# Kernel optimization log

Measured on AMD Instinct MI355X. Metric: run time of the kernel, lower is better.

Reference implementation:

```python
import jax, jax.numpy as jnp
import numpy as np

B, N, E, D, OUT, L = 4, 10000, 160000, 128, 64, 4
NEG = 0.01  # LeakyReLU slope

def lrelu(x):
    return jnp.where(x > 0, x, NEG * x)

def setup_inputs() -> dict:
    key = jax.random.key(0)
    ks = jax.random.split(key, 20)
    s = 0.05
    inp = {
        "x": jax.random.normal(ks[0], (B, N * 3), dtype=jnp.float32),
        "edge_index": jax.random.randint(ks[1], (2, E), 0, N, dtype=jnp.int32),
        # f0: Linear(3, D)
        "w0": jax.random.normal(ks[2], (3, D), dtype=jnp.float32) * s,
        "b0": jax.random.normal(ks[3], (D,), dtype=jnp.float32) * s,
        # per-layer params stacked on leading L axis
        "ew1": jax.random.normal(ks[4], (L, 2 * D + 1, D), dtype=jnp.float32) * s,
        "eb1": jax.random.normal(ks[5], (L, D), dtype=jnp.float32) * s,
        "ew2": jax.random.normal(ks[6], (L, D, D), dtype=jnp.float32) * s,
        "eb2": jax.random.normal(ks[7], (L, D), dtype=jnp.float32) * s,
        "cw": jax.random.normal(ks[8], (L, D, 1), dtype=jnp.float32) * s,
        "cb": jax.random.normal(ks[9], (L, 1), dtype=jnp.float32) * s,
        "nw1": jax.random.normal(ks[10], (L, 2 * D, D), dtype=jnp.float32) * s,
        "nb1": jax.random.normal(ks[11], (L, D), dtype=jnp.float32) * s,
        "nw2": jax.random.normal(ks[12], (L, D, D), dtype=jnp.float32) * s,
        "nb2": jax.random.normal(ks[13], (L, D), dtype=jnp.float32) * s,
        # project: Linear(D, OUT)
        "wp": jax.random.normal(ks[14], (D, OUT), dtype=jnp.float32) * s,
        "bp": jax.random.normal(ks[15], (OUT,), dtype=jnp.float32) * s,
    }
    return inp

def reference(x, edge_index, w0, b0, ew1, eb1, ew2, eb2, cw, cb, nw1, nb1, nw2, nb2, wp, bp):
    b = x.shape[0]
    n = x.shape[1] // 3
    pos = x.reshape(b, n, 3)            # coordinates [B,N,3]
    h = lrelu(pos @ w0 + b0)            # node features [B,N,D]
    row, col = edge_index[0], edge_index[1]
    # per-node in-edge counts (same for all layers/batches); scatter_mean -> 0 for empty nodes
    cnt = jnp.zeros((n,), x.dtype).at[col].add(1.0)
    denom = jnp.maximum(cnt, 1.0)[None, :, None]
    for i in range(L):
        rel = pos[:, row] - pos[:, col]                          # [B,E,3]
        dist_sq = jnp.sum(rel * rel, axis=-1, keepdims=True)     # [B,E,1]
        edge_in = jnp.concatenate([h[:, row], h[:, col], dist_sq], axis=-1)  # [B,E,2D+1]
        msg = lrelu(lrelu(edge_in @ ew1[i] + eb1[i]) @ ew2[i] + eb2[i])       # [B,E,D]
        aggr = jnp.zeros((b, n, msg.shape[-1]), msg.dtype).at[:, col].add(msg) / denom  # scatter_mean
        coord_update = jnp.tanh(aggr @ cw[i] + cb[i])            # [B,N,1]
        pos = pos + coord_update * 0.1
        node_in = jnp.concatenate([h, aggr], axis=-1)            # [B,N,2D]
        h = h + lrelu(lrelu(node_in @ nw1[i] + nb1[i]) @ nw2[i] + nb2[i])
    return lrelu(h.mean(axis=1) @ wp + bp)                       # [B,OUT]
```

## Files before the change

### kernel.cpp

```cpp
#include <hip/hip_runtime.h>
#include <hip/hip_bf16.h>
#include <math.h>

#define BB   4
#define NN   10000
#define NP   10112
#define EE   160000
#define DD   128
#define OUTD 64
#define LL   4
#define NEGS 0.01f
#define MSTR 136
#define RSF  68

typedef __attribute__((ext_vector_type(8))) short   short8;
typedef __attribute__((ext_vector_type(4))) float   floatx4;
typedef __attribute__((ext_vector_type(4))) uint    uintx4;

__device__ __forceinline__ float lrelu(float x) { return fmaxf(x, NEGS * x); }
__device__ __forceinline__ ushort f2bf(float x) {
    uint u = __builtin_bit_cast(uint, x);
    return (ushort)((u + 0x7FFFu + ((u >> 16) & 1u)) >> 16);
}
__device__ __forceinline__ float bf2f(ushort u) {
    uint v = ((uint)u) << 16;
    return __builtin_bit_cast(float, v);
}
__device__ __forceinline__ float bcf(uint u) { return __builtin_bit_cast(float, u); }

__global__ void k_cvtw_all(const float* __restrict__ ew1, const float* __restrict__ ew2,
                           const float* __restrict__ nw1, const float* __restrict__ nw2,
                           ushort* __restrict__ wtopf, ushort* __restrict__ wmidf,
                           ushort* __restrict__ ew2f, ushort* __restrict__ nw1f,
                           ushort* __restrict__ nw2f) {
    int tid = blockIdx.x * 256 + threadIdx.x;
    const float* src; ushort* dst; int pitch, nks, loc;
    if (tid < 8192)       { src = ew1;                     dst = wtopf; pitch = 257; nks = 4; loc = tid; }
    else if (tid < 16384) { src = ew1 + (size_t)128 * DD;  dst = wmidf; pitch = 257; nks = 4; loc = tid - 8192; }
    else if (tid < 24576) { src = ew2;                     dst = ew2f;  pitch = 128; nks = 4; loc = tid - 16384; }
    else if (tid < 40960) { src = nw1;                     dst = nw1f;  pitch = 256; nks = 8; loc = tid - 24576; }
    else                  { src = nw2;                     dst = nw2f;  pitch = 128; nks = 4; loc = tid - 40960; }
    int lane = loc & 63;
    int nt   = (loc >> 6) & 7;
    int ks   = (loc >> 9) % nks;
    int l    = loc / (nks * 512);
    int quad = lane >> 4, l16 = lane & 15;
    int n = nt * 16 + l16;
    const float* s = src + (size_t)l * pitch * DD;
    ushort* d = dst + (size_t)loc * 8;
    #pragma unroll
    for (int j = 0; j < 8; ++j)
        d[j] = f2bf(s[(size_t)(ks * 32 + quad * 8 + j) * DD + n]);
}

__global__ void k_h0(const float* __restrict__ x, const float* __restrict__ w0,
                     const float* __restrict__ b0, ushort* __restrict__ hb) {
    int idx = blockIdx.x * 256 + threadIdx.x;
    if (idx >= BB * NP * DD) return;
    int d  = idx & (DD - 1);
    int bn = idx >> 7;
    int n  = bn % NP, b = bn / NP;
    float v = 0.0f;
    if (n < NN) {
        const float* p = x + ((size_t)b * NN + n) * 3;
        v = lrelu(b0[d] + p[0] * w0[d] + p[1] * w0[DD + d] + p[2] * w0[2 * DD + d]);
    }
    hb[idx] = f2bf(v);
}

__global__ void k_count(const int* __restrict__ col, float* __restrict__ cnt,
                        int* __restrict__ ecnt) {
    int e = blockIdx.x * blockDim.x + threadIdx.x;
    if (e < EE) {
        int c = col[e];
        atomicAdd(&cnt[c], 1.0f);
        atomicAdd(&ecnt[c], 1);
    }
}

__global__ __launch_bounds__(256) void k_scan(const int* __restrict__ ecnt,
                                              int* __restrict__ cursor) {
    __shared__ int s_sum[256];
    int t = threadIdx.x;
    int base = t * 40;
    int s = 0;
    for (int i = 0; i < 40; ++i) {
        int n = base + i;
        if (n < NN) s += ecnt[n];
    }
    s_sum[t] = s;
    __syncthreads();
    if (t == 0) {
        int a = 0;
        for (int i = 0; i < 256; ++i) { int v = s_sum[i]; s_sum[i] = a; a += v; }
    }
    __syncthreads();
    int a = s_sum[t];
    for (int i = 0; i < 40; ++i) {
        int n = base + i;
        if (n < NN) { cursor[n] = a; a += ecnt[n]; }
    }
}

__global__ void k_place(const int* __restrict__ row, const int* __restrict__ col,
                        int* __restrict__ cursor,
                        int* __restrict__ rowS, int* __restrict__ colS) {
    int e = blockIdx.x * blockDim.x + threadIdx.x;
    if (e >= EE) return;
    int c = col[e];
    int p = atomicAdd(&cursor[c], 1);
    rowS[p] = row[e];
    colS[p] = c;
}

__global__ __launch_bounds__(256) void k_pq(
    const ushort* __restrict__ hb, const ushort* __restrict__ wtf,
    const ushort* __restrict__ wmf, const float* __restrict__ b1,
    ushort* __restrict__ P, ushort* __restrict__ Q)
{
    __shared__ __align__(16) ushort s_out[64 * MSTR];
    const int g = blockIdx.x;
    const int b = (g >> 1) & 3;
    const int n0 = ((g >> 3) * 2 + (g & 1)) * 64;
    const int t = threadIdx.x;
    const int w = t >> 6, lane = t & 63, quad = lane >> 4, l16 = lane & 15;
    const int rw = w * 16;
    const int nw = n0 + rw;

    const ushort* hptr = hb + ((size_t)b * NP + nw + l16) * DD;
    float b1r[8];
    #pragma unroll
    for (int nt = 0; nt < 8; ++nt) b1r[nt] = b1[nt * 16 + l16];

    const short8* wt = (const short8*)wtf;
    const short8* wm = (const short8*)wmf;

    #pragma unroll
    for (int pass = 0; pass < 2; ++pass) {
        floatx4 ap[8];
        #pragma unroll
        for (int nt = 0; nt < 8; ++nt)
            #pragma unroll
            for (int r = 0; r < 4; ++r) ap[nt][r] = pass ? b1r[nt] : 0.0f;
        const short8* wv = pass ? wm : wt;
        #pragma unroll
        for (int ks = 0; ks < 4; ++ks) {
            short8 bf[8];
            #pragma unroll
            for (int nt = 0; nt < 8; ++nt) bf[nt] = wv[(ks * 8 + nt) * 64 + lane];
            short8 af = *(const short8*)(hptr + ks * 32 + quad * 8);
            #pragma unroll
            for (int nt = 0; nt < 8; ++nt)
                ap[nt] = __builtin_amdgcn_mfma_f32_16x16x32_bf16(af, bf[nt], ap[nt], 0, 0, 0);
        }
        #pragma unroll
        for (int nt = 0; nt < 8; ++nt)
            #pragma unroll
            for (int r = 0; r < 4; ++r)
                s_out[(rw + quad * 4 + r) * MSTR + nt * 16 + l16] = f2bf(ap[nt][r]);
        ushort* dst = pass ? Q : P;
        #pragma unroll
        for (int i = 0; i < 4; ++i) {
            int row = rw + i * 4 + quad;
            short8 v = *(const short8*)&s_out[row * MSTR + l16 * 8];
            *(short8*)(dst + ((size_t)b * NP + n0 + row) * DD + l16 * 8) = v;
        }
    }
}

__global__ __launch_bounds__(256, 4) void k_edge(
    const float* __restrict__ pos,
    const ushort* __restrict__ P, const ushort* __restrict__ Q,
    const int* __restrict__ rowS, const int* __restrict__ colS,
    const float* __restrict__ w1last,
    const ushort* __restrict__ w2f, const float* __restrict__ b2,
    float* __restrict__ aggr)
{
    __shared__ int    s_row[128];
    __shared__ int    s_col[128];
    __shared__ float  s_ds[128];
    __shared__ float  s_red[128 * RSF];

    const int g    = blockIdx.x;
    const int b    = (g >> 1) & 3;
    const int tile = (g >> 3) * 2 + (g & 1);
    const int e0   = tile * 128;
    const int t    = threadIdx.x;
    const int w    = t >> 6, lane = t & 63;
    const int quad = lane >> 4, l16 = lane & 15;

    if (t < 128) {
        int e = e0 + t;
        int r = rowS[e], c = colS[e];
        s_row[t] = r;
        s_col[t] = c;
        const float* pr = pos + ((size_t)b * NN + r) * 3;
        const float* pc = pos + ((size_t)b * NN + c) * 3;
        float dx = pr[0] - pc[0], dy = pr[1] - pc[1], dz = pr[2] - pc[2];
        s_ds[t] = dx * dx + dy * dy + dz * dz;
    }
    __syncthreads();

    const int ew = w * 32;
    const ushort* pp[2];
    const ushort* qp[2];
    float dsv[2];
    #pragma unroll
    for (int mt = 0; mt < 2; ++mt) {
        int el = ew + mt * 16 + l16;
        pp[mt]  = P + ((size_t)b * NP + s_row[el]) * DD;
        qp[mt]  = Q + ((size_t)b * NP + s_col[el]) * DD;
        dsv[mt] = s_ds[el];
    }

    uintx4 pf[2][4], qf[2][4];
    #pragma unroll
    for (int ks = 0; ks < 4; ++ks) {
        const int koff = ks * 32 + quad * 8;
        #pragma unroll
        for (int mt = 0; mt < 2; ++mt) {
            pf[mt][ks] = *(const uintx4*)(pp[mt] + koff);
            qf[mt][ks] = *(const uintx4*)(qp[mt] + koff);
        }
    }

    uintx4 mid[2][4];
    #pragma unroll
    for (int ks = 0; ks < 4; ++ks) {
        const int koff = ks * 32 + quad * 8;
        floatx4 wl0 = *(const floatx4*)(w1last + koff);
        floatx4 wl1 = *(const floatx4*)(w1last + koff + 4);
        float wl[8] = {wl0[0], wl0[1], wl0[2], wl0[3], wl1[0], wl1[1], wl1[2], wl1[3]};
        #pragma unroll
        for (int mt = 0; mt < 2; ++mt) {
            #pragma unroll
            for (int i = 0; i < 4; ++i) {
                uint pv = pf[mt][ks][i], qv = qf[mt][ks][i];
                float vlo = lrelu(bcf(pv << 16) + bcf(qv << 16) + dsv[mt] * wl[2 * i]);
                float vhi = lrelu(bcf(pv & 0xFFFF0000u) + bcf(qv & 0xFFFF0000u) + dsv[mt] * wl[2 * i + 1]);
                mid[mt][ks][i] = (__builtin_bit_cast(uint, vlo) >> 16) |
                                 (__builtin_bit_cast(uint, vhi) & 0xFFFF0000u);
            }
        }
    }

    float b2r[8];
    #pragma unroll
    for (int nt = 0; nt < 8; ++nt) b2r[nt] = b2[nt * 16 + l16];

    const short8* w2v = (const short8*)w2f;
    #pragma unroll
    for (int ph = 0; ph < 2; ++ph) {
        floatx4 acc[2][4];
        #pragma unroll
        for (int mt = 0; mt < 2; ++mt)
            #pragma unroll
            for (int ntl = 0; ntl < 4; ++ntl)
                #pragma unroll
                for (int r = 0; r < 4; ++r) acc[mt][ntl][r] = b2r[ph * 4 + ntl];

        #pragma unroll
        for (int ks = 0; ks < 4; ++ks) {
            short8 bf[4];
            #pragma unroll
            for (int ntl = 0; ntl < 4; ++ntl)
                bf[ntl] = w2v[(ks * 8 + ph * 4 + ntl) * 64 + lane];
            #pragma unroll
            for (int mt = 0; mt < 2; ++mt) {
                short8 af = __builtin_bit_cast(short8, mid[mt][ks]);
                #pragma unroll
                for (int ntl = 0; ntl < 4; ++ntl)
                    acc[mt][ntl] = __builtin_amdgcn_mfma_f32_16x16x32_bf16(af, bf[ntl], acc[mt][ntl], 0, 0, 0);
            }
        }

        #pragma unroll
        for (int mt = 0; mt < 2; ++mt)
            #pragma unroll
            for (int ntl = 0; ntl < 4; ++ntl)
                #pragma unroll
                for (int r = 0; r < 4; ++r)
                    s_red[(ew + mt * 16 + quad * 4 + r) * RSF + ntl * 16 + l16] =
                        lrelu(acc[mt][ntl][r]);

        const int d = ph * 64 + lane;
        float run = 0.0f;
        int prev = s_col[ew];
        for (int r = 0; r < 32; ++r) {
            int cid = s_col[ew + r];
            float v = s_red[(ew + r) * RSF + lane];
            if (cid != prev) {
                atomicAdd(&aggr[((size_t)b * NP + prev) * DD + d], run);
                run = 0.0f;
                prev = cid;
            }
            run += v;
        }
        atomicAdd(&aggr[((size_t)b * NP + prev) * DD + d], run);
    }
}

__global__ __launch_bounds__(256) void k_node(
    ushort* hb, float* aggr, const float* __restrict__ cnt,
    const float* __restrict__ cw, const float* __restrict__ cb,
    const ushort* __restrict__ w1f, const float* __restrict__ b1,
    const ushort* __restrict__ w2f, const float* __restrict__ b2,
    float* __restrict__ pos,
    int do_pq,
    const ushort* __restrict__ wtn, const ushort* __restrict__ wmn,
    const float* __restrict__ b1n,
    ushort* __restrict__ P, ushort* __restrict__ Q)
{
    __shared__ __align__(16) ushort s_mid[64 * MSTR];
    __shared__ __align__(16) ushort s_ho[64 * MSTR];

    const int g    = blockIdx.x;
    const int b    = (g >> 1) & 3;
    const int n0   = ((g >> 3) * 2 + (g & 1)) * 64;
    const int t    = threadIdx.x;
    const int w    = t >> 6, lane = t & 63;
    const int quad = lane >> 4, l16 = lane & 15;
    const int rw   = w * 16;
    const int nw   = n0 + rw;

    #pragma unroll
    for (int i = 0; i < 4; ++i) {
        int row = rw + i * 4 + quad;
        short8 v = *(const short8*)(hb + ((size_t)b * NP + n0 + row) * DD + l16 * 8);
        *(short8*)&s_ho[row * MSTR + l16 * 8] = v;
    }

    float* aptr = aggr + ((size_t)b * NP + nw + l16) * DD;
    float inv = 0.0f;
    {
        int node = nw + l16;
        if (node < NN) { float dn = cnt[node]; inv = 1.0f / fmaxf(dn, 1.0f); }
    }
    float b1r[8], b2r[8];
    #pragma unroll
    for (int nt = 0; nt < 8; ++nt) {
        int d = nt * 16 + l16;
        b1r[nt] = b1[d]; b2r[nt] = b2[d];
    }

    floatx4 acc[8];
    #pragma unroll
    for (int nt = 0; nt < 8; ++nt)
        #pragma unroll
        for (int r = 0; r < 4; ++r) acc[nt][r] = b1r[nt];

    float cwacc = 0.0f;
    const floatx4 zero4 = {0.0f, 0.0f, 0.0f, 0.0f};
    const short8* w1v = (const short8*)w1f;
    #pragma unroll
    for (int ks = 0; ks < 8; ++ks) {
        short8 bf[8];
        #pragma unroll
        for (int nt = 0; nt < 8; ++nt) bf[nt] = w1v[(ks * 8 + nt) * 64 + lane];
        const int koff = (ks & 3) * 32 + quad * 8;
        if (ks < 4) {
            short8 af = *(const short8*)(&s_ho[(rw + l16) * MSTR + koff]);
            #pragma unroll
            for (int nt = 0; nt < 8; ++nt)
                acc[nt] = __builtin_amdgcn_mfma_f32_16x16x32_bf16(af, bf[nt], acc[nt], 0, 0, 0);
        } else {
            floatx4 cw0 = *(const floatx4*)(cw + koff);
            floatx4 cw1 = *(const floatx4*)(cw + koff + 4);
            floatx4 a0 = *(const floatx4*)(aptr + koff);
            floatx4 a1 = *(const floatx4*)(aptr + koff + 4);
            *(floatx4*)(aptr + koff)     = zero4;
            *(floatx4*)(aptr + koff + 4) = zero4;
            short8 af;
            #pragma unroll
            for (int j = 0; j < 4; ++j) {
                float v = a0[j] * inv;
                af[j] = (short)f2bf(v);
                cwacc += v * cw0[j];
            }
            #pragma unroll
            for (int j = 0; j < 4; ++j) {
                float v = a1[j] * inv;
                af[4 + j] = (short)f2bf(v);
                cwacc += v * cw1[j];
            }
            #pragma unroll
            for (int nt = 0; nt < 8; ++nt)
                acc[nt] = __builtin_amdgcn_mfma_f32_16x16x32_bf16(af, bf[nt], acc[nt], 0, 0, 0);
        }
    }

    {
        float full = cwacc;
        full += __shfl_xor(full, 16);
        full += __shfl_xor(full, 32);
        int node = nw + l16;
        if (quad == 0 && node < NN) {
            float cu = 0.1f * tanhf(full + cb[0]);
            float* pp = pos + ((size_t)b * NN + node) * 3;
            pp[0] += cu; pp[1] += cu; pp[2] += cu;
        }
    }

    #pragma unroll
    for (int nt = 0; nt < 8; ++nt)
        #pragma unroll
        for (int r = 0; r < 4; ++r)
            s_mid[(rw + quad * 4 + r) * MSTR + nt * 16 + l16] = f2bf(lrelu(acc[nt][r]));

    floatx4 acc2[8];
    #pragma unroll
    for (int nt = 0; nt < 8; ++nt)
        #pragma unroll
        for (int r = 0; r < 4; ++r) acc2[nt][r] = b2r[nt];

    const short8* w2v = (const short8*)w2f;
    #pragma unroll
    for (int ks = 0; ks < 4; ++ks) {
        short8 bf[8];
        #pragma unroll
        for (int nt = 0; nt < 8; ++nt) bf[nt] = w2v[(ks * 8 + nt) * 64 + lane];
        short8 af = *(const short8*)(&s_mid[(rw + l16) * MSTR + ks * 32 + quad * 8]);
        #pragma unroll
        for (int nt = 0; nt < 8; ++nt)
            acc2[nt] = __builtin_amdgcn_mfma_f32_16x16x32_bf16(af, bf[nt], acc2[nt], 0, 0, 0);
    }

    #pragma unroll
    for (int nt = 0; nt < 8; ++nt)
        #pragma unroll
        for (int r = 0; r < 4; ++r) {
            int row = rw + quad * 4 + r;
            float hold = bf2f(s_ho[row * MSTR + nt * 16 + l16]);
            float hv = hold + lrelu(acc2[nt][r]);
            s_mid[row * MSTR + nt * 16 + l16] = f2bf(hv);
        }

    #pragma unroll
    for (int i = 0; i < 4; ++i) {
        int row = rw + i * 4 + quad;
        int n = n0 + row;
        short8 v = *(const short8*)&s_mid[row * MSTR + l16 * 8];
        if (n < NN)
            *(short8*)(hb + ((size_t)b * NP + n) * DD + l16 * 8) = v;
    }

    if (do_pq) {
        const short8* wt = (const short8*)wtn;
        const short8* wm = (const short8*)wmn;
        float b1nr[8];
        #pragma unroll
        for (int nt = 0; nt < 8; ++nt) b1nr[nt] = b1n[nt * 16 + l16];

        #pragma unroll
        for (int pass = 0; pass < 2; ++pass) {
            floatx4 ap[8];
            #pragma unroll
            for (int nt = 0; nt < 8; ++nt)
                #pragma unroll
                for (int r = 0; r < 4; ++r) ap[nt][r] = pass ? b1nr[nt] : 0.0f;
            const short8* wv = pass ? wm : wt;
            #pragma unroll
            for (int ks = 0; ks < 4; ++ks) {
                short8 bf[8];
                #pragma unroll
                for (int nt = 0; nt < 8; ++nt) bf[nt] = wv[(ks * 8 + nt) * 64 + lane];
                short8 af = *(const short8*)(&s_mid[(rw + l16) * MSTR + ks * 32 + quad * 8]);
                #pragma unroll
                for (int nt = 0; nt < 8; ++nt)
                    ap[nt] = __builtin_amdgcn_mfma_f32_16x16x32_bf16(af, bf[nt], ap[nt], 0, 0, 0);
            }
            #pragma unroll
            for (int nt = 0; nt < 8; ++nt)
                #pragma unroll
                for (int r = 0; r < 4; ++r)
                    s_ho[(rw + quad * 4 + r) * MSTR + nt * 16 + l16] = f2bf(ap[nt][r]);
            ushort* dst = pass ? Q : P;
            #pragma unroll
            for (int i = 0; i < 4; ++i) {
                int row = rw + i * 4 + quad;
                short8 v = *(const short8*)&s_ho[row * MSTR + l16 * 8];
                *(short8*)(dst + ((size_t)b * NP + n0 + row) * DD + l16 * 8) = v;
            }
        }
    }
}

#define NPC 50
__global__ void k_mean(const ushort* __restrict__ hb, float* __restrict__ hm) {
    int b  = blockIdx.y;
    int n0 = blockIdx.x * NPC;
    int d  = threadIdx.x;
    float s = 0.0f;
    for (int n = n0; n < n0 + NPC; ++n) s += bf2f(hb[((size_t)b * NP + n) * DD + d]);
    atomicAdd(&hm[b * DD + d], s);
}

__global__ void k_proj(const float* __restrict__ hm, const float* __restrict__ wp,
                       const float* __restrict__ bp, float* __restrict__ out) {
    int t = threadIdx.x;
    int b = t >> 6, o = t & (OUTD - 1);
    float s = 0.0f;
    for (int d2 = 0; d2 < DD; ++d2) s += hm[b * DD + d2] * wp[d2 * OUTD + o];
    s = s * (1.0f / NN) + bp[o];
    out[b * OUTD + o] = lrelu(s);
}

extern "C" void kernel_launch(void* const* d_in, const int* in_sizes, int n_in,
                              void* d_out, int out_size, void* d_ws, size_t ws_size,
                              hipStream_t stream) {
    (void)in_sizes; (void)n_in; (void)out_size; (void)ws_size;
    const float* x   = (const float*)d_in[0];
    const int*   ei  = (const int*)d_in[1];
    const float* w0  = (const float*)d_in[2];
    const float* b0  = (const float*)d_in[3];
    const float* ew1 = (const float*)d_in[4];
    const float* eb1 = (const float*)d_in[5];
    const float* ew2 = (const float*)d_in[6];
    const float* eb2 = (const float*)d_in[7];
    const float* cw  = (const float*)d_in[8];
    const float* cb  = (const float*)d_in[9];
    const float* nw1 = (const float*)d_in[10];
    const float* nb1 = (const float*)d_in[11];
    const float* nw2 = (const float*)d_in[12];
    const float* nb2 = (const float*)d_in[13];
    const float* wp  = (const float*)d_in[14];
    const float* bp  = (const float*)d_in[15];
    const int* row = ei;
    const int* col = ei + EE;

    const size_t HSZ = (size_t)BB * NP * DD;
    float* ws   = (float*)d_ws;
    float* aggr = ws;
    float* pos  = aggr + HSZ;
    float* cnt  = pos + (size_t)BB * NN * 3;
    float* hm   = cnt + NN;
    ushort* hb    = (ushort*)(hm + 512);
    ushort* Pb    = hb + HSZ;
    ushort* Qb    = Pb + HSZ;
    ushort* wtopf = Qb + HSZ;
    ushort* wmidf = wtopf + (size_t)LL * 16384;
    ushort* ew2f  = wmidf + (size_t)LL * 16384;
    ushort* nw1f  = ew2f + (size_t)LL * 16384;
    ushort* nw2f  = nw1f + (size_t)LL * 32768;
    int* ecnt   = (int*)(nw2f + (size_t)LL * 16384);
    int* cursor = ecnt + NN;
    int* rowS   = cursor + NN;
    int* colS   = rowS + EE;

    hipMemcpyAsync(pos, x, sizeof(float) * (size_t)BB * NN * 3,
                   hipMemcpyDeviceToDevice, stream);
    hipMemsetAsync(cnt, 0, sizeof(float) * NN, stream);
    hipMemsetAsync(ecnt, 0, sizeof(int) * NN, stream);
    hipMemsetAsync(hm, 0, sizeof(float) * BB * DD, stream);
    hipMemsetAsync(aggr, 0, sizeof(float) * HSZ, stream);

    k_cvtw_all<<<192, 256, 0, stream>>>(ew1, ew2, nw1, nw2,
                                        wtopf, wmidf, ew2f, nw1f, nw2f);

    k_h0<<<((int)HSZ + 255) / 256, 256, 0, stream>>>(x, w0, b0, hb);
    k_count<<<(EE + 255) / 256, 256, 0, stream>>>(col, cnt, ecnt);
    k_scan<<<1, 256, 0, stream>>>(ecnt, cursor);
    k_place<<<(EE + 255) / 256, 256, 0, stream>>>(row, col, cursor, rowS, colS);

    k_pq<<<(NP / 64) * BB, 256, 0, stream>>>(hb, wtopf, wmidf, eb1, Pb, Qb);

    for (int i = 0; i < LL; ++i) {
        k_edge<<<(EE / 128) * BB, 256, 0, stream>>>(
            pos, Pb, Qb, rowS, colS,
            ew1 + (size_t)i * 257 * DD + (size_t)256 * DD,
            ew2f + (size_t)i * 16384,
            eb2 + (size_t)i * DD,
            aggr);
        int nx = (i < LL - 1) ? (i + 1) : i;
        k_node<<<(NP / 64) * BB, 256, 0, stream>>>(
            hb, aggr, cnt,
            cw + (size_t)i * DD, cb + i,
            nw1f + (size_t)i * 32768, nb1 + (size_t)i * DD,
            nw2f + (size_t)i * 16384, nb2 + (size_t)i * DD,
            pos,
            (i < LL - 1) ? 1 : 0,
            wtopf + (size_t)nx * 16384, wmidf + (size_t)nx * 16384,
            eb1 + (size_t)nx * DD,
            Pb, Qb);
    }

    k_mean<<<dim3(NN / NPC, BB), DD, 0, stream>>>(hb, hm);
    k_proj<<<1, 256, 0, stream>>>(hm, wp, bp, (float*)d_out);
}
```

Before: 589.7 us.

## Halve edge-kernel reduction LDS buffer and split segmented scatter across half-waves

```diff
diff --git a/kernel.cpp b/kernel.cpp
--- a/kernel.cpp
+++ b/kernel.cpp
@@ -11,7 +11,7 @@
 #define LL   4
 #define NEGS 0.01f
 #define MSTR 136
-#define RSF  68
+#define RSF  34
 
 typedef __attribute__((ext_vector_type(8))) short   short8;
 typedef __attribute__((ext_vector_type(4))) float   floatx4;
@@ -168,7 +168,7 @@
     }
 }
 
-__global__ __launch_bounds__(256, 4) void k_edge(
+__global__ __launch_bounds__(256, 8) void k_edge(
     const float* __restrict__ pos,
     const ushort* __restrict__ P, const ushort* __restrict__ Q,
     const int* __restrict__ rowS, const int* __restrict__ colS,
@@ -176,10 +176,10 @@
     const ushort* __restrict__ w2f, const float* __restrict__ b2,
     float* __restrict__ aggr)
 {
-    __shared__ int    s_row[128];
-    __shared__ int    s_col[128];
-    __shared__ float  s_ds[128];
-    __shared__ float  s_red[128 * RSF];
+    __shared__ __align__(16) int    s_row[128];
+    __shared__ __align__(16) int    s_col[128];
+    __shared__ __align__(16) float  s_ds[128];
+    __shared__ __align__(16) float  s_red[128 * RSF];
 
     const int g    = blockIdx.x;
     const int b    = (g >> 1) & 3;
@@ -202,6 +202,22 @@
     __syncthreads();
 
     const int ew = w * 32;
+
+    const int rh    = lane >> 5;
+    const int colL  = lane & 31;
+    const int rbase = ew + rh * 16;
+    int bmask = 0, cid0;
+    {
+        const int4* cp = (const int4*)(&s_col[rbase]);
+        int4 ca = cp[0], cb = cp[1], cc4 = cp[2], cd = cp[3];
+        int cc[16] = {ca.x, ca.y, ca.z, ca.w, cb.x, cb.y, cb.z, cb.w,
+                      cc4.x, cc4.y, cc4.z, cc4.w, cd.x, cd.y, cd.z, cd.w};
+        cid0 = cc[0];
+        #pragma unroll
+        for (int r2 = 1; r2 < 16; ++r2)
+            if (cc[r2] != cc[r2 - 1]) bmask |= (1 << r2);
+    }
+
     const ushort* pp[2];
     const ushort* qp[2];
     float dsv[2];
@@ -238,26 +254,28 @@
                 uint pv = pf[mt][ks][i], qv = qf[mt][ks][i];
                 float vlo = lrelu(bcf(pv << 16) + bcf(qv << 16) + dsv[mt] * wl[2 * i]);
                 float vhi = lrelu(bcf(pv & 0xFFFF0000u) + bcf(qv & 0xFFFF0000u) + dsv[mt] * wl[2 * i + 1]);
-                mid[mt][ks][i] = (__builtin_bit_cast(uint, vlo) >> 16) |
-                                 (__builtin_bit_cast(uint, vhi) & 0xFFFF0000u);
+                mid[mt][ks][i] = __builtin_amdgcn_perm(
+                    __builtin_bit_cast(uint, vhi), __builtin_bit_cast(uint, vlo), 0x07060302u);
             }
         }
     }
 
-    float b2r[8];
-    #pragma unroll
-    for (int nt = 0; nt < 8; ++nt) b2r[nt] = b2[nt * 16 + l16];
+    float* aggr_bd = aggr + (size_t)b * NP * DD;
 
     const short8* w2v = (const short8*)w2f;
     #pragma unroll
     for (int ph = 0; ph < 2; ++ph) {
+        float b2r4[4];
+        #pragma unroll
+        for (int ntl = 0; ntl < 4; ++ntl) b2r4[ntl] = b2[(ph * 4 + ntl) * 16 + l16];
+
         floatx4 acc[2][4];
         #pragma unroll
         for (int mt = 0; mt < 2; ++mt)
             #pragma unroll
             for (int ntl = 0; ntl < 4; ++ntl)
                 #pragma unroll
-                for (int r = 0; r < 4; ++r) acc[mt][ntl][r] = b2r[ph * 4 + ntl];
+                for (int r = 0; r < 4; ++r) acc[mt][ntl][r] = b2r4[ntl];
 
         #pragma unroll
         for (int ks = 0; ks < 4; ++ks) {
@@ -275,28 +293,34 @@
         }
 
         #pragma unroll
-        for (int mt = 0; mt < 2; ++mt)
-            #pragma unroll
-            for (int ntl = 0; ntl < 4; ++ntl)
+        for (int sp = 0; sp < 2; ++sp) {
+            #pragma unroll
+            for (int mt = 0; mt < 2; ++mt)
                 #pragma unroll
-                for (int r = 0; r < 4; ++r)
-                    s_red[(ew + mt * 16 + quad * 4 + r) * RSF + ntl * 16 + l16] =
-                        lrelu(acc[mt][ntl][r]);
-
-        const int d = ph * 64 + lane;
-        float run = 0.0f;
-        int prev = s_col[ew];
-        for (int r = 0; r < 32; ++r) {
-            int cid = s_col[ew + r];
-            float v = s_red[(ew + r) * RSF + lane];
-            if (cid != prev) {
-                atomicAdd(&aggr[((size_t)b * NP + prev) * DD + d], run);
-                run = 0.0f;
-                prev = cid;
+                for (int j = 0; j < 2; ++j) {
+                    const int ntl = sp * 2 + j;
+                    #pragma unroll
+                    for (int r = 0; r < 4; ++r)
+                        s_red[(ew + mt * 16 + quad * 4 + r) * RSF + j * 16 + l16] =
+                            lrelu(acc[mt][ntl][r]);
+                }
+
+            const int d = ph * 64 + sp * 32 + colL;
+            float* ab = aggr_bd + d;
+            float run = 0.0f;
+            int cid = cid0;
+            #pragma unroll
+            for (int r = 0; r < 16; ++r) {
+                float v = s_red[(rbase + r) * RSF + colL];
+                if (bmask & (1 << r)) {
+                    atomicAdd(ab + (size_t)cid * DD, run);
+                    run = 0.0f;
+                    cid = s_col[rbase + r];
+                }
+                run += v;
             }
-            run += v;
-        }
-        atomicAdd(&aggr[((size_t)b * NP + prev) * DD + d], run);
+            atomicAdd(ab + (size_t)cid * DD, run);
+        }
     }
 }
 
```

Measured after the change: 1.279 ms. +116.9%, slower.
